# Kernel optimization log

Hardware: AMD Instinct MI355X
Metric: run time of the kernel (lower is better)

## Reference

```python
import jax, jax.numpy as jnp
import numpy as np

UNITS = 1024
LEVELS = 16
CHUNK = UNITS // LEVELS  # 64


def cumsoftmax(x, mode):
    # softmax then cumsum along last axis; 'r2l' reverses before/after
    if mode == 'l2r':
        return jnp.cumsum(jax.nn.softmax(x, axis=-1), axis=-1)
    else:  # 'r2l'
        xr = x[..., ::-1]
        return jnp.cumsum(jax.nn.softmax(xr, axis=-1), axis=-1)[..., ::-1]


def setup_inputs() -> dict:
    key = jax.random.key(0)
    k1, k2, k3 = jax.random.split(key, 3)
    B, T, D = 32, 512, 1024
    G = UNITS * 4 + LEVELS * 2  # 4128
    x = jax.random.normal(k1, (B, T, D), dtype=jnp.float32)
    kernel = jax.random.normal(k2, (D, G), dtype=jnp.float32) * (1.0 / np.sqrt(D))
    recurrent_kernel = jax.random.normal(k3, (UNITS, G), dtype=jnp.float32) * (1.0 / np.sqrt(UNITS))
    bias = jnp.zeros((G,), dtype=jnp.float32)
    return {"x": x, "kernel": kernel, "recurrent_kernel": recurrent_kernel, "bias": bias}


def reference(x, kernel, recurrent_kernel, bias):
    B, T, D = x.shape
    L, U, C = LEVELS, UNITS, CHUNK

    def one_step(carry, x_t):
        c_last, h_last = carry  # [B, U] each
        z = x_t @ kernel + h_last @ recurrent_kernel + bias  # [B, 4U+2L]
        f_master = cumsoftmax(z[:, :L], 'l2r')[:, :, None]       # [B, L, 1]
        i_master = cumsoftmax(z[:, L:2 * L], 'r2l')[:, :, None]  # [B, L, 1]
        g = z[:, 2 * L:].reshape(B, 4 * L, C)
        f_gate = jax.nn.sigmoid(g[:, :L])
        i_gate = jax.nn.sigmoid(g[:, L:2 * L])
        o_gate = jax.nn.sigmoid(g[:, 2 * L:3 * L])
        c_in = jnp.tanh(g[:, 3 * L:])
        c_prev = c_last.reshape(B, L, C)
        overlap = f_master * i_master
        c_out = (overlap * (f_gate * c_prev + i_gate * c_in)
                 + (f_master - overlap) * c_prev
                 + (i_master - overlap) * c_in)
        h_out = (o_gate * jnp.tanh(c_out)).reshape(B, U)
        c_out = c_out.reshape(B, U)
        return (c_out, h_out), h_out

    init = (jnp.zeros((B, U), x.dtype), jnp.zeros((B, U), x.dtype))
    _, h_seq = jax.lax.scan(one_step, init, jnp.swapaxes(x, 0, 1))  # [T, B, U]
    return jnp.swapaxes(h_seq, 0, 1)  # [B, T, U] (return_sequences=True)
```

## Files before the change

kernel.cpp:

```cpp
#include <hip/hip_runtime.h>

#define TT 512
#define GG 4128
#define GPAD 4224
#define NBLK2 64
#define NTHR2 512

typedef _Float16 f16;
typedef _Float16 half8 __attribute__((ext_vector_type(8)));
typedef _Float16 half4 __attribute__((ext_vector_type(4)));
typedef float f32x4 __attribute__((ext_vector_type(4)));
typedef unsigned u32x4 __attribute__((ext_vector_type(4)));
typedef unsigned long long ull;

__device__ __forceinline__ half8 h8(uint4 v) {
  union { uint4 u; half8 h; } c; c.u = v; return c.h;
}

__device__ __forceinline__ u32x4 ld_cohx4(const unsigned* p) {
  u32x4 r;
  asm volatile("global_load_dwordx4 %0, %1, off sc0 sc1"
               : "=v"(r) : "v"(p) : "memory");
  return r;
}

__global__ void k_transpose_cvt(const float* __restrict__ in, f16* __restrict__ out,
                                int R, int C) {
  __shared__ float tile[32][33];
  int bx = blockIdx.x * 32, by = blockIdx.y * 32;
  int tx = threadIdx.x & 31, ty = threadIdx.x >> 5;
#pragma unroll
  for (int j = 0; j < 4; ++j) {
    int r = by + ty + j * 8;
    tile[ty + j * 8][tx] = in[(long)r * C + bx + tx];
  }
  __syncthreads();
#pragma unroll
  for (int j = 0; j < 4; ++j) {
    int c = bx + ty + j * 8;
    out[(long)c * R + by + tx] = (f16)tile[tx][ty + j * 8];
  }
}

__global__ __launch_bounds__(256) void k_gemm_xw(
    const float* __restrict__ X,
    const f16* __restrict__ Bt,
    const float* __restrict__ bias,
    f16* __restrict__ Zm,
    f16* __restrict__ Zg) {
  __shared__ f16 As[128 * 32];
  __shared__ f16 Bs[128 * 32];
  const int m0 = blockIdx.x * 128;
  const int n0 = blockIdx.y * 128;
  const int tid = threadIdx.x;
  const int wave = tid >> 6, lane = tid & 63;
  const int mrow = (wave & 1) * 64, ncol = (wave >> 1) * 64;
  f32x4 acc[4][4];
#pragma unroll
  for (int i = 0; i < 4; ++i)
#pragma unroll
    for (int j = 0; j < 4; ++j)
      acc[i][j] = (f32x4){0.f, 0.f, 0.f, 0.f};

  float4 ra[4];
  uint4 rb[2];
  auto load_tiles = [&](int k0) {
#pragma unroll
    for (int q = 0; q < 4; ++q) {
      int flat = q * 256 + tid;
      int r = flat >> 3, s = flat & 7;
      ra[q] = *(const float4*)(X + (long)(m0 + r) * 1024 + k0 + s * 4);
    }
#pragma unroll
    for (int q = 0; q < 2; ++q) {
      int flat = q * 256 + tid;
      int r = flat >> 2, s = flat & 3;
      rb[q] = *(const uint4*)(Bt + (long)(n0 + r) * 1024 + k0 + s * 8);
    }
  };
  load_tiles(0);
  for (int kt = 0; kt < 32; ++kt) {
    __syncthreads();
#pragma unroll
    for (int q = 0; q < 4; ++q) {
      int flat = q * 256 + tid;
      half4 h;
      h[0] = (f16)ra[q].x; h[1] = (f16)ra[q].y;
      h[2] = (f16)ra[q].z; h[3] = (f16)ra[q].w;
      *(half4*)((char*)As + flat * 8) = h;
    }
#pragma unroll
    for (int q = 0; q < 2; ++q) {
      int flat = q * 256 + tid;
      *(uint4*)((char*)Bs + flat * 16) = rb[q];
    }
    __syncthreads();
    if (kt + 1 < 32) load_tiles((kt + 1) * 32);
    const int kseg2 = ((lane >> 4) * 8) * 2;
    half8 af[4], bf[4];
#pragma unroll
    for (int i = 0; i < 4; ++i) {
      int r = mrow + i * 16 + (lane & 15);
      af[i] = *(const half8*)((const char*)As + r * 64 + kseg2);
      int c = ncol + i * 16 + (lane & 15);
      bf[i] = *(const half8*)((const char*)Bs + c * 64 + kseg2);
    }
#pragma unroll
    for (int i = 0; i < 4; ++i)
#pragma unroll
      for (int j = 0; j < 4; ++j)
        acc[i][j] = __builtin_amdgcn_mfma_f32_16x16x32_f16(af[i], bf[j], acc[i][j], 0, 0, 0);
  }
#pragma unroll
  for (int j = 0; j < 4; ++j) {
    int n = n0 + ncol + j * 16 + (lane & 15);
    if (n < GG) {
      float bv = bias[n];
      const int isM = (n < 32);
      int q = 0, u4 = 0, g2 = 0;
      if (!isM) {
        int k = n - 32;
        q = k >> 10;
        int u = k & 1023;
        g2 = u >> 4;
        u4 = u & 15;
      }
#pragma unroll
      for (int i = 0; i < 4; ++i) {
#pragma unroll
        for (int r = 0; r < 4; ++r) {
          int m = m0 + mrow + i * 16 + (lane >> 4) * 4 + r;
          int b = m >> 9, tt2 = m & 511;
          f16 v = (f16)(acc[i][j][r] + bv);
          if (isM)
            Zm[((long)(tt2 * 32 + b)) * 32 + n] = v;
          else
            Zg[((((long)tt2 * 64 + g2) * 32 + b) * 16 + u4) * 4 + q] = v;
        }
      }
    }
  }
}

__device__ __forceinline__ float sigm(float x) { return 1.f / (1.f + __expf(-x)); }
__device__ __forceinline__ float tanh_(float x) {
  float ax = fabsf(x);
  float e = __expf(-2.f * ax);
  float t = (1.f - e) / (1.f + e);
  return copysignf(t, x);
}
#define AG_ST(p, v) __hip_atomic_store((p), (v), __ATOMIC_RELAXED, __HIP_MEMORY_SCOPE_AGENT)

__device__ __forceinline__ void bar_lds() {
  asm volatile("s_waitcnt lgkmcnt(0)" ::: "memory");
  __builtin_amdgcn_sched_barrier(0);
  __builtin_amdgcn_s_barrier();
  __builtin_amdgcn_sched_barrier(0);
}

__global__ __launch_bounds__(NTHR2, 2) void k_onlstm(
    const f16* __restrict__ Zm, const f16* __restrict__ Zg,
    const f16* __restrict__ Rt, unsigned* __restrict__ hbuf32,
    float* __restrict__ Y) {
  extern __shared__ char lds[];
  float* cumlds = (float*)(lds + 32768);
  const int g = blockIdx.x, tid = threadIdx.x;
  const int wave = tid >> 6, lane = tid & 63;
  const int lr = lane & 15, lq = lane >> 4;
  const int kq = wave;
  const int b = tid >> 4;
  const int u = tid & 15;
  const int L0 = g >> 2;
  const int side = tid >> 5, mb = tid & 31;

  uint4 bq[16], bm[8];
  {
    const f16* base = Rt + (long)kq * 128 + lq * 8;
#pragma unroll
    for (int q = 0; q < 4; ++q)
#pragma unroll
      for (int ks = 0; ks < 4; ++ks)
        bq[q * 4 + ks] = *(const uint4*)(base + (long)(32 + q * 1024 + g * 16 + lr) * 1024 + ks * 32);
#pragma unroll
    for (int ct = 0; ct < 2; ++ct)
#pragma unroll
      for (int ks = 0; ks < 4; ++ks)
        bm[ct * 4 + ks] = *(const uint4*)(base + (long)(ct * 16 + lr) * 1024 + ks * 32);
#pragma unroll
    for (int i = 0; i < 16; ++i)
      asm volatile("" : "+v"(bq[i].x), "+v"(bq[i].y), "+v"(bq[i].z), "+v"(bq[i].w));
#pragma unroll
    for (int i = 0; i < 8; ++i)
      asm volatile("" : "+v"(bm[i].x), "+v"(bm[i].y), "+v"(bm[i].z), "+v"(bm[i].w));
  }
  float creg = 0.f;

  for (int t = 0; t < TT; ++t) {
    half4 zxh = *(const half4*)(Zg + ((((long)t * 64 + g) * 32 + b) * 16 + u) * 4);
    half8 zmr0, zmr1;
    if (wave == 0) {
      const half8* zmp = (const half8*)(Zm + ((long)t * 32 + mb) * 32 + side * 16);
      zmr0 = zmp[0];
      zmr1 = zmp[1];
    }
    const unsigned* hb = hbuf32 + (t & 1) * 32768;
    const unsigned tg = (unsigned)(t & 0xFF);
    u32x4 hw[16];
    for (;;) {
#pragma unroll
      for (int it = 0; it < 16; ++it)
        hw[it] = ld_cohx4(hb + (it * 512 + tid) * 4);
      asm volatile("s_waitcnt vmcnt(0)" ::: "memory");
      __builtin_amdgcn_sched_barrier(0);
      unsigned bad = 0;
#pragma unroll
      for (int it = 0; it < 16; ++it)
        bad |= (hw[it].x ^ tg) | (hw[it].y ^ tg) | (hw[it].z ^ tg) | (hw[it].w ^ tg);
      if (__all((int)((bad & 0xFFu) == 0u))) break;
    }
#pragma unroll
    for (int it = 0; it < 16; ++it) {
      int idx = it * 512 + tid;
      int bb = idx >> 8, j8 = idx & 255;
      half4 hh;
      hh[0] = (f16)__uint_as_float(hw[it].x);
      hh[1] = (f16)__uint_as_float(hw[it].y);
      hh[2] = (f16)__uint_as_float(hw[it].z);
      hh[3] = (f16)__uint_as_float(hw[it].w);
      *(half4*)(lds + ((bb * 128 + ((j8 >> 1) ^ (bb & 7))) << 4) + (j8 & 1) * 8) = hh;
    }
    bar_lds();
    f32x4 acc[4][2], accm[2][2];
#pragma unroll
    for (int q = 0; q < 4; ++q) {
      acc[q][0] = (f32x4){0.f, 0.f, 0.f, 0.f};
      acc[q][1] = (f32x4){0.f, 0.f, 0.f, 0.f};
    }
#pragma unroll
    for (int ct = 0; ct < 2; ++ct) {
      accm[ct][0] = (f32x4){0.f, 0.f, 0.f, 0.f};
      accm[ct][1] = (f32x4){0.f, 0.f, 0.f, 0.f};
    }
#pragma unroll
    for (int ks = 0; ks < 4; ++ks) {
      int ch = kq * 16 + ks * 4 + lq;
      half8 a0 = *(const half8*)(lds + ((lr * 128 + (ch ^ (lr & 7))) << 4));
      half8 a1 = *(const half8*)(lds + (((16 + lr) * 128 + (ch ^ ((16 + lr) & 7))) << 4));
#pragma unroll
      for (int q = 0; q < 4; ++q) {
        acc[q][0] = __builtin_amdgcn_mfma_f32_16x16x32_f16(a0, h8(bq[q * 4 + ks]), acc[q][0], 0, 0, 0);
        acc[q][1] = __builtin_amdgcn_mfma_f32_16x16x32_f16(a1, h8(bq[q * 4 + ks]), acc[q][1], 0, 0, 0);
      }
#pragma unroll
      for (int ct = 0; ct < 2; ++ct) {
        accm[ct][0] = __builtin_amdgcn_mfma_f32_16x16x32_f16(a0, h8(bm[ct * 4 + ks]), accm[ct][0], 0, 0, 0);
        accm[ct][1] = __builtin_amdgcn_mfma_f32_16x16x32_f16(a1, h8(bm[ct * 4 + ks]), accm[ct][1], 0, 0, 0);
      }
    }
#pragma unroll
    for (int q = 0; q < 4; ++q)
#pragma unroll
      for (int bt = 0; bt < 2; ++bt) {
        int bsw = (bt * 16 + lq * 4) ^ ((lr & 7) << 2);
        *(f32x4*)(lds + 65536 + (((kq * 64 + q * 16 + lr) * 32 + bsw) << 2)) = acc[q][bt];
      }
    bar_lds();
#pragma unroll
    for (int ct = 0; ct < 2; ++ct)
#pragma unroll
      for (int bt = 0; bt < 2; ++bt) {
        int col = ct * 16 + lr;
        int bsw = (bt * 16 + lq * 4) ^ ((col & 7) << 2);
        *(f32x4*)(lds + (((kq * 32 + col) * 32 + bsw) << 2)) = accm[ct][bt];
      }
    float z[4];
#pragma unroll
    for (int q = 0; q < 4; ++q) {
      float s = 0.f;
      int bsw = b ^ ((u & 7) << 2);
#pragma unroll
      for (int k8 = 0; k8 < 8; ++k8)
        s += *(const float*)(lds + 65536 + (((k8 * 64 + q * 16 + u) * 32 + bsw) << 2));
      z[q] = s + (float)zxh[q];
    }
    float f = sigm(z[0]), i_ = sigm(z[1]), o = sigm(z[2]);
    float ci = tanh_(z[3]);
    bar_lds();
    if (wave == 0) {
      float v[16];
#pragma unroll
      for (int j = 0; j < 16; ++j) {
        int col = side * 16 + j;
        int bsw = mb ^ ((col & 7) << 2);
        float s = 0.f;
#pragma unroll
        for (int k8 = 0; k8 < 8; ++k8)
          s += *(const float*)(lds + (((k8 * 32 + col) * 32 + bsw) << 2));
        v[j] = s + (float)((j < 8) ? zmr0[j] : zmr1[j - 8]);
      }
      float mx = v[0];
#pragma unroll
      for (int j = 1; j < 16; ++j) mx = fmaxf(mx, v[j]);
      float ssum = 0.f, p = 0.f;
#pragma unroll
      for (int j = 0; j < 16; ++j) {
        float e = __expf(v[j] - mx);
        ssum += e;
        bool take = side ? (j >= L0) : (j <= L0);
        if (take) p += e;
      }
      cumlds[side * 32 + mb] = p / ssum;
    }
    bar_lds();
    float fm = cumlds[b], im = cumlds[32 + b];
    float ov = fm * im;
    float cn = ov * (f * creg + i_ * ci) + (fm - ov) * creg + (im - ov) * ci;
    creg = cn;
    float hval = o * tanh_(cn);
    unsigned hword = (__float_as_uint(hval) & 0xFFFFFF00u) | ((unsigned)(t + 1) & 0xFFu);
    AG_ST(hbuf32 + ((t + 1) & 1) * 32768 + b * 1024 + g * 16 + u, hword);
    Y[((long)b * TT + t) * 1024 + g * 16 + u] = hval;
  }
}

extern "C" void kernel_launch(void* const* d_in, const int* in_sizes, int n_in,
                              void* d_out, int out_size, void* d_ws, size_t ws_size,
                              hipStream_t stream) {
  const float* X = (const float*)d_in[0];
  const float* W = (const float*)d_in[1];
  const float* Rm = (const float*)d_in[2];
  const float* bias = (const float*)d_in[3];
  float* Y = (float*)d_out;
  char* ws = (char*)d_ws;

  const size_t off_h = 0;
  const size_t off_Zm = 262144;
  const size_t off_Wt = 1310720;
  const size_t off_Rt = 9961472;
  const size_t off_Zg = 18415616;
  const size_t need = off_Zg + (size_t)TT * 64 * 32 * 16 * 4 * 2;
  if (ws_size < need) return;

  unsigned* hbuf32 = (unsigned*)(ws + off_h);
  f16* Zm = (f16*)(ws + off_Zm);
  f16* Wt = (f16*)(ws + off_Wt);
  f16* Rt = (f16*)(ws + off_Rt);
  f16* Zg = (f16*)(ws + off_Zg);

  hipMemsetAsync(ws + off_h, 0, 262144, stream);
  hipMemsetAsync(ws + off_Wt + (size_t)GG * 1024 * 2, 0, (size_t)(GPAD - GG) * 1024 * 2, stream);

  k_transpose_cvt<<<dim3(129, 32), 256, 0, stream>>>(W, Wt, 1024, GG);
  k_transpose_cvt<<<dim3(129, 32), 256, 0, stream>>>(Rm, Rt, 1024, GG);
  k_gemm_xw<<<dim3(128, 33), 256, 0, stream>>>(X, Wt, bias, Zm, Zg);

  hipFuncSetAttribute((const void*)k_onlstm, hipFuncAttributeMaxDynamicSharedMemorySize, 131072);
  k_onlstm<<<NBLK2, NTHR2, 131072, stream>>>(Zm, Zg, Rt, hbuf32, Y);
}
```

Before: 3.833 ms.

## Pack hidden state as fp16 pairs with 64-bit tags and add per-wave flag polling

Each pair of hidden values is now published as two fp16s packed with a full 32-bit step tag in one 64-bit atomic store, replacing one 32-bit store per value whose low byte held the tag. A per-block, per-wave flag array gives waiting blocks a cheaper spin target before they re-read the full h buffer. The master-gate recurrent GEMM is also redistributed so each wave computes one column tile over a quarter of K instead of two tiles over an eighth, which halves the master reduction loads. These changes cut polling traffic and per-step synchronisation latency; the costs are extra flag stores and a different interleaving between flag and data visibility.

```diff
diff --git a/kernel.cpp b/kernel.cpp
--- a/kernel.cpp
+++ b/kernel.cpp
@@ -150,6 +150,7 @@
   return copysignf(t, x);
 }
 #define AG_ST(p, v) __hip_atomic_store((p), (v), __ATOMIC_RELAXED, __HIP_MEMORY_SCOPE_AGENT)
+#define AG_ST8(p, v) __hip_atomic_store((p), (v), __ATOMIC_RELAXED, __HIP_MEMORY_SCOPE_AGENT)
 
 __device__ __forceinline__ void bar_lds() {
   asm volatile("s_waitcnt lgkmcnt(0)" ::: "memory");
@@ -160,14 +161,16 @@
 
 __global__ __launch_bounds__(NTHR2, 2) void k_onlstm(
     const f16* __restrict__ Zm, const f16* __restrict__ Zg,
-    const f16* __restrict__ Rt, unsigned* __restrict__ hbuf32,
-    float* __restrict__ Y) {
+    const f16* __restrict__ Rt, ull* __restrict__ hbuf8,
+    unsigned* __restrict__ flagbuf, float* __restrict__ Y) {
   extern __shared__ char lds[];
   float* cumlds = (float*)(lds + 32768);
   const int g = blockIdx.x, tid = threadIdx.x;
   const int wave = tid >> 6, lane = tid & 63;
   const int lr = lane & 15, lq = lane >> 4;
   const int kq = wave;
+  const int kh = wave >> 1, ct = wave & 1;
+  const int colm = ct * 16 + lr;
   const int b = tid >> 4;
   const int u = tid & 15;
   const int L0 = g >> 2;
@@ -175,17 +178,16 @@
 
   uint4 bq[16], bm[8];
   {
-    const f16* base = Rt + (long)kq * 128 + lq * 8;
+    const f16* baseg = Rt + (long)kq * 128 + lq * 8;
 #pragma unroll
     for (int q = 0; q < 4; ++q)
 #pragma unroll
       for (int ks = 0; ks < 4; ++ks)
-        bq[q * 4 + ks] = *(const uint4*)(base + (long)(32 + q * 1024 + g * 16 + lr) * 1024 + ks * 32);
-#pragma unroll
-    for (int ct = 0; ct < 2; ++ct)
-#pragma unroll
-      for (int ks = 0; ks < 4; ++ks)
-        bm[ct * 4 + ks] = *(const uint4*)(base + (long)(ct * 16 + lr) * 1024 + ks * 32);
+        bq[q * 4 + ks] = *(const uint4*)(baseg + (long)(32 + q * 1024 + g * 16 + lr) * 1024 + ks * 32);
+    const f16* basem = Rt + (long)colm * 1024 + kh * 256 + lq * 8;
+#pragma unroll
+    for (int ks = 0; ks < 8; ++ks)
+      bm[ks] = *(const uint4*)(basem + ks * 32);
 #pragma unroll
     for (int i = 0; i < 16; ++i)
       asm volatile("" : "+v"(bq[i].x), "+v"(bq[i].y), "+v"(bq[i].z), "+v"(bq[i].w));
@@ -203,8 +205,8 @@
       zmr0 = zmp[0];
       zmr1 = zmp[1];
     }
-    const unsigned* hb = hbuf32 + (t & 1) * 32768;
-    const unsigned tg = (unsigned)(t & 0xFF);
+    const unsigned* hb = (const unsigned*)(hbuf8 + (t & 1) * 16384);
+    const unsigned tg = (unsigned)t;
     u32x4 hw[16];
     for (;;) {
 #pragma unroll
@@ -215,32 +217,39 @@
       unsigned bad = 0;
 #pragma unroll
       for (int it = 0; it < 16; ++it)
-        bad |= (hw[it].x ^ tg) | (hw[it].y ^ tg) | (hw[it].z ^ tg) | (hw[it].w ^ tg);
-      if (__all((int)((bad & 0xFFu) == 0u))) break;
+        bad |= (hw[it].y ^ tg) | (hw[it].w ^ tg);
+      if (__all((int)(bad == 0u))) break;
+      {
+        const unsigned* fb = flagbuf + lane * 8;
+        for (;;) {
+          u32x4 f0 = ld_cohx4(fb);
+          u32x4 f1 = ld_cohx4(fb + 4);
+          asm volatile("s_waitcnt vmcnt(0)" ::: "memory");
+          unsigned mn = f0.x;
+          mn = mn < f0.y ? mn : f0.y; mn = mn < f0.z ? mn : f0.z;
+          mn = mn < f0.w ? mn : f0.w; mn = mn < f1.x ? mn : f1.x;
+          mn = mn < f1.y ? mn : f1.y; mn = mn < f1.z ? mn : f1.z;
+          mn = mn < f1.w ? mn : f1.w;
+          if (__all((int)(mn >= tg))) break;
+        }
+      }
     }
 #pragma unroll
     for (int it = 0; it < 16; ++it) {
       int idx = it * 512 + tid;
       int bb = idx >> 8, j8 = idx & 255;
-      half4 hh;
-      hh[0] = (f16)__uint_as_float(hw[it].x);
-      hh[1] = (f16)__uint_as_float(hw[it].y);
-      hh[2] = (f16)__uint_as_float(hw[it].z);
-      hh[3] = (f16)__uint_as_float(hw[it].w);
-      *(half4*)(lds + ((bb * 128 + ((j8 >> 1) ^ (bb & 7))) << 4) + (j8 & 1) * 8) = hh;
+      ull word = ((ull)hw[it].z << 32) | (ull)hw[it].x;
+      *(ull*)(lds + (((bb * 128 + ((j8 >> 1) ^ (bb & 7))) << 4) + (j8 & 1) * 8)) = word;
     }
     bar_lds();
-    f32x4 acc[4][2], accm[2][2];
+    f32x4 acc[4][2], accm0, accm1;
 #pragma unroll
     for (int q = 0; q < 4; ++q) {
       acc[q][0] = (f32x4){0.f, 0.f, 0.f, 0.f};
       acc[q][1] = (f32x4){0.f, 0.f, 0.f, 0.f};
     }
-#pragma unroll
-    for (int ct = 0; ct < 2; ++ct) {
-      accm[ct][0] = (f32x4){0.f, 0.f, 0.f, 0.f};
-      accm[ct][1] = (f32x4){0.f, 0.f, 0.f, 0.f};
-    }
+    accm0 = (f32x4){0.f, 0.f, 0.f, 0.f};
+    accm1 = accm0;
 #pragma unroll
     for (int ks = 0; ks < 4; ++ks) {
       int ch = kq * 16 + ks * 4 + lq;
@@ -251,11 +260,14 @@
         acc[q][0] = __builtin_amdgcn_mfma_f32_16x16x32_f16(a0, h8(bq[q * 4 + ks]), acc[q][0], 0, 0, 0);
         acc[q][1] = __builtin_amdgcn_mfma_f32_16x16x32_f16(a1, h8(bq[q * 4 + ks]), acc[q][1], 0, 0, 0);
       }
-#pragma unroll
-      for (int ct = 0; ct < 2; ++ct) {
-        accm[ct][0] = __builtin_amdgcn_mfma_f32_16x16x32_f16(a0, h8(bm[ct * 4 + ks]), accm[ct][0], 0, 0, 0);
-        accm[ct][1] = __builtin_amdgcn_mfma_f32_16x16x32_f16(a1, h8(bm[ct * 4 + ks]), accm[ct][1], 0, 0, 0);
-      }
+    }
+#pragma unroll
+    for (int ks = 0; ks < 8; ++ks) {
+      int chm = kh * 32 + ks * 4 + lq;
+      half8 a0 = *(const half8*)(lds + ((lr * 128 + (chm ^ (lr & 7))) << 4));
+      half8 a1 = *(const half8*)(lds + (((16 + lr) * 128 + (chm ^ ((16 + lr) & 7))) << 4));
+      accm0 = __builtin_amdgcn_mfma_f32_16x16x32_f16(a0, h8(bm[ks]), accm0, 0, 0, 0);
+      accm1 = __builtin_amdgcn_mfma_f32_16x16x32_f16(a1, h8(bm[ks]), accm1, 0, 0, 0);
     }
 #pragma unroll
     for (int q = 0; q < 4; ++q)
@@ -266,13 +278,10 @@
       }
     bar_lds();
 #pragma unroll
-    for (int ct = 0; ct < 2; ++ct)
-#pragma unroll
-      for (int bt = 0; bt < 2; ++bt) {
-        int col = ct * 16 + lr;
-        int bsw = (bt * 16 + lq * 4) ^ ((col & 7) << 2);
-        *(f32x4*)(lds + (((kq * 32 + col) * 32 + bsw) << 2)) = accm[ct][bt];
-      }
+    for (int bt = 0; bt < 2; ++bt) {
+      int bsw = (bt * 16 + lq * 4) ^ ((colm & 7) << 2);
+      *(f32x4*)(lds + (((kh * 32 + colm) * 32 + bsw) << 2)) = (bt ? accm1 : accm0);
+    }
     float z[4];
 #pragma unroll
     for (int q = 0; q < 4; ++q) {
@@ -294,8 +303,8 @@
         int bsw = mb ^ ((col & 7) << 2);
         float s = 0.f;
 #pragma unroll
-        for (int k8 = 0; k8 < 8; ++k8)
-          s += *(const float*)(lds + (((k8 * 32 + col) * 32 + bsw) << 2));
+        for (int k4 = 0; k4 < 4; ++k4)
+          s += *(const float*)(lds + (((k4 * 32 + col) * 32 + bsw) << 2));
         v[j] = s + (float)((j < 8) ? zmr0[j] : zmr1[j - 8]);
       }
       float mx = v[0];
@@ -317,8 +326,15 @@
     float cn = ov * (f * creg + i_ * ci) + (fm - ov) * creg + (im - ov) * ci;
     creg = cn;
     float hval = o * tanh_(cn);
-    unsigned hword = (__float_as_uint(hval) & 0xFFFFFF00u) | ((unsigned)(t + 1) & 0xFFu);
-    AG_ST(hbuf32 + ((t + 1) & 1) * 32768 + b * 1024 + g * 16 + u, hword);
+    float hp = __shfl_xor(hval, 1);
+    if (!(u & 1)) {
+      union { f16 h[2]; unsigned w; } pk;
+      pk.h[0] = (f16)hval;
+      pk.h[1] = (f16)hp;
+      ull word = (ull)pk.w | ((ull)(unsigned)(t + 1) << 32);
+      AG_ST8(hbuf8 + ((t + 1) & 1) * 16384 + b * 512 + g * 8 + (u >> 1), word);
+    }
+    if (lane == 0) AG_ST(flagbuf + g * 8 + wave, (unsigned)(t + 1));
     Y[((long)b * TT + t) * 1024 + g * 16 + u] = hval;
   }
 }
@@ -333,21 +349,23 @@
   float* Y = (float*)d_out;
   char* ws = (char*)d_ws;
 
-  const size_t off_h = 0;
-  const size_t off_Zm = 262144;
-  const size_t off_Wt = 1310720;
-  const size_t off_Rt = 9961472;
-  const size_t off_Zg = 18415616;
+  const size_t off_flags = 0;
+  const size_t off_h = 4096;
+  const size_t off_Zm = 266240;
+  const size_t off_Wt = 1314816;
+  const size_t off_Rt = 9965568;
+  const size_t off_Zg = 18419712;
   const size_t need = off_Zg + (size_t)TT * 64 * 32 * 16 * 4 * 2;
   if (ws_size < need) return;
 
-  unsigned* hbuf32 = (unsigned*)(ws + off_h);
+  unsigned* flagbuf = (unsigned*)(ws + off_flags);
+  ull* hbuf8 = (ull*)(ws + off_h);
   f16* Zm = (f16*)(ws + off_Zm);
   f16* Wt = (f16*)(ws + off_Wt);
   f16* Rt = (f16*)(ws + off_Rt);
   f16* Zg = (f16*)(ws + off_Zg);
 
-  hipMemsetAsync(ws + off_h, 0, 262144, stream);
+  hipMemsetAsync(ws, 0, 266240, stream);
   hipMemsetAsync(ws + off_Wt + (size_t)GG * 1024 * 2, 0, (size_t)(GPAD - GG) * 1024 * 2, stream);
 
   k_transpose_cvt<<<dim3(129, 32), 256, 0, stream>>>(W, Wt, 1024, GG);
@@ -355,5 +373,5 @@
   k_gemm_xw<<<dim3(128, 33), 256, 0, stream>>>(X, Wt, bias, Zm, Zg);
 
   hipFuncSetAttribute((const void*)k_onlstm, hipFuncAttributeMaxDynamicSharedMemorySize, 131072);
-  k_onlstm<<<NBLK2, NTHR2, 131072, stream>>>(Zm, Zg, Rt, hbuf32, Y);
-}
+  k_onlstm<<<NBLK2, NTHR2, 131072, stream>>>(Zm, Zg, Rt, hbuf8, flagbuf, Y);
+}
```

Measured after the change: 4.151 ms. 8.3% more time.
